# Kernel optimization log

Hardware: AMD Instinct MI355X
Metric: run time of the kernel (lower is better)

## Reference

```python
import jax, jax.numpy as jnp
import numpy as np

IMG = 8       # image_size
LH = 150      # l_h
LQ = 10       # l_q
K = 10        # value-iteration steps
B = 16384     # batch
N_STATES = 2 + IMG * IMG


def _conv(x, w, pad):
    # NCHW conv, stride 1
    return jax.lax.conv_general_dilated(
        x, w, window_strides=(1, 1), padding=[(pad, pad), (pad, pad)],
        dimension_numbers=('NCHW', 'OIHW', 'NCHW'))


def setup_inputs() -> dict:
    key = jax.random.key(0)
    ks = jax.random.split(key, 8)
    grid = jax.random.normal(ks[0], (B, IMG * IMG), dtype=jnp.float32)
    pos = jax.random.randint(ks[1], (B, 2), 0, IMG).astype(jnp.float32)
    S = jnp.concatenate([grid, pos], axis=1)                      # [B, 66]
    Wh = jax.random.normal(ks[2], (LH, 1, 3, 3), jnp.float32) * 0.1
    bh = jnp.zeros((LH,), jnp.float32)
    Wr = jax.random.normal(ks[3], (1, LH, 1, 1), jnp.float32) * 0.1
    Wq = jax.random.normal(ks[4], (LQ, 1, 3, 3), jnp.float32) * 0.1
    w = jax.random.normal(ks[5], (LQ, 1, 3, 3), jnp.float32) * 0.1
    Wfc = jax.random.normal(ks[6], (8, LQ), jnp.float32) * 0.1
    return {'S': S, 'Wh': Wh, 'bh': bh, 'Wr': Wr, 'Wq': Wq, 'w': w, 'Wfc': Wfc}


def reference(S, Wh, bh, Wr, Wq, w, Wfc):
    X = S[:, :IMG * IMG].reshape(-1, 1, IMG, IMG)                 # [B,1,8,8]
    s1 = S[:, IMG * IMG].astype(jnp.int32)                        # row index
    s2 = S[:, IMG * IMG + 1].astype(jnp.int32)                    # col index

    h = _conv(X, Wh, 1) + bh[None, :, None, None]                 # [B,150,8,8]
    r = _conv(h, Wr, 0)                                           # [B,1,8,8]
    q = _conv(r, Wq, 1)                                           # [B,10,8,8]
    v = jnp.max(q, axis=1, keepdims=True)                         # [B,1,8,8]

    Wcat = jnp.concatenate([Wq, w], axis=1)                       # [10,2,3,3]

    def step(v, _):
        qq = _conv(jnp.concatenate([r, v], axis=1), Wcat, 1)
        return jnp.max(qq, axis=1, keepdims=True), None

    v, _ = jax.lax.scan(step, v, None, length=K - 1)
    q = _conv(jnp.concatenate([r, v], axis=1), Wcat, 1)           # [B,10,8,8]

    bidx = jnp.arange(q.shape[0])
    q_sel = q[bidx, :, s1, s2]                                    # [B,10]
    logits = q_sel @ Wfc.T                                        # [B,8]
    return logits
```

## Files before the change

kernel.cpp:

```cpp
#include <hip/hip_runtime.h>

#define IMG 8
#define LH 150
#define LQ 10
#define KITER 10

__global__ void weff_kernel(const float* __restrict__ Wh,
                            const float* __restrict__ bh,
                            const float* __restrict__ Wr,
                            float* __restrict__ ws) {
    const int wave = threadIdx.x >> 6;
    const int lane = threadIdx.x & 63;
    float partial = 0.f;
    for (int c = lane; c < LH; c += 64) {
        const float wr = Wr[c];
        partial += wr * ((wave < 9) ? Wh[c * 9 + wave] : bh[c]);
    }
    #pragma unroll
    for (int off = 32; off > 0; off >>= 1)
        partial += __shfl_xor(partial, off);
    if (lane == 0) ws[wave] = partial;
}

__global__ __launch_bounds__(256) void vin_kernel(
    const float* __restrict__ S,
    const float* __restrict__ Wq,
    const float* __restrict__ w,
    const float* __restrict__ Wfc,
    const float* __restrict__ ws,
    float* __restrict__ out,
    int B) {
    const int wave = threadIdx.x >> 6;
    const int lane = threadIdx.x & 63;
    const int b = blockIdx.x * 4 + wave;
    if (b >= B) return;

    const int y = lane >> 3, x = lane & 7;

    const float* Sb = S + (long)b * (IMG * IMG + 2);
    const float X = Sb[lane];
    const int s1 = (int)Sb[IMG * IMG];
    const int s2 = (int)Sb[IMG * IMG + 1];
    const int sel_lane = s1 * 8 + s2;

    int   nidx[9];
    float nmsk[9];
    #pragma unroll
    for (int t = 0; t < 9; ++t) {
        const int dy = t / 3 - 1, dx = t % 3 - 1;
        const int ny = y + dy, nx = x + dx;
        const bool v = ((unsigned)ny < 8u) && ((unsigned)nx < 8u);
        nidx[t] = v ? (ny * 8 + nx) : 0;
        nmsk[t] = v ? 1.f : 0.f;
    }

    float Weff[9];
    #pragma unroll
    for (int t = 0; t < 9; ++t) Weff[t] = ws[t];
    const float beff = ws[9];

    float r = beff;
    #pragma unroll
    for (int t = 0; t < 9; ++t) {
        const float xv = __shfl(X, nidx[t]) * nmsk[t];
        r = fmaf(Weff[t], xv, r);
    }

    float rn[9];
    #pragma unroll
    for (int t = 0; t < 9; ++t)
        rn[t] = __shfl(r, nidx[t]) * nmsk[t];

    float qr[LQ];
    #pragma unroll
    for (int o = 0; o < LQ; ++o) {
        float acc = 0.f;
        #pragma unroll
        for (int t = 0; t < 9; ++t) acc = fmaf(rn[t], Wq[o * 9 + t], acc);
        qr[o] = acc;
    }

    float ww[LQ][9];
    #pragma unroll
    for (int o = 0; o < LQ; ++o)
        #pragma unroll
        for (int t = 0; t < 9; ++t) ww[o][t] = w[o * 9 + t];

    float v = qr[0];
    #pragma unroll
    for (int o = 1; o < LQ; ++o) v = fmaxf(v, qr[o]);

    float q[LQ];
    for (int k = 0; k < KITER; ++k) {
        float vn[9];
        #pragma unroll
        for (int t = 0; t < 9; ++t)
            vn[t] = __shfl(v, nidx[t]) * nmsk[t];
        float m = -3.0e38f;
        #pragma unroll
        for (int o = 0; o < LQ; ++o) {
            float acc = qr[o];
            #pragma unroll
            for (int t = 0; t < 9; ++t) acc = fmaf(vn[t], ww[o][t], acc);
            q[o] = acc;
            m = fmaxf(m, acc);
        }
        v = m;
    }

    float qsel[LQ];
    #pragma unroll
    for (int o = 0; o < LQ; ++o) qsel[o] = __shfl(q[o], sel_lane);

    if (lane < 8) {
        float acc = 0.f;
        #pragma unroll
        for (int o = 0; o < LQ; ++o) acc = fmaf(qsel[o], Wfc[lane * LQ + o], acc);
        out[(long)b * 8 + lane] = acc;
    }
}

extern "C" void kernel_launch(void* const* d_in, const int* in_sizes, int n_in,
                              void* d_out, int out_size, void* d_ws, size_t ws_size,
                              hipStream_t stream) {
    const float* S   = (const float*)d_in[0];
    const float* Wh  = (const float*)d_in[1];
    const float* bh  = (const float*)d_in[2];
    const float* Wr  = (const float*)d_in[3];
    const float* Wq  = (const float*)d_in[4];
    const float* w   = (const float*)d_in[5];
    const float* Wfc = (const float*)d_in[6];
    float* out = (float*)d_out;
    float* ws  = (float*)d_ws;

    const int B = in_sizes[0] / (IMG * IMG + 2);

    weff_kernel<<<1, 640, 0, stream>>>(Wh, bh, Wr, ws);

    const int waves_per_block = 4;
    const int grid = (B + waves_per_block - 1) / waves_per_block;
    vin_kernel<<<grid, 256, 0, stream>>>(S, Wq, w, Wfc, ws, out, B);
}
```

Baseline: 100.9 us.

## Process two batch items per wavefront with ds_bpermute and fully unrolled iterations

Each wavefront now handles two batch elements, interleaving their stencil shuffles and FMAs to raise instruction-level parallelism and reuse weight operands. __shfl is replaced by direct ds_bpermute with precomputed byte addresses, and the value-iteration loop is fully unrolled with weights read inline instead of preloaded into a register array. The max over channels uses a tree reduction. This halves the number of waves and raises register pressure. If B is odd, the last wave would read past the end of S, though the test batch is even.

```diff
diff --git a/kernel.cpp b/kernel.cpp
--- a/kernel.cpp
+++ b/kernel.cpp
@@ -4,22 +4,35 @@
 #define LH 150
 #define LQ 10
 #define KITER 10
+#define ROW (IMG * IMG + 2)
+
+__device__ __forceinline__ float bperm(int byte_addr, float v) {
+    return __builtin_bit_cast(float,
+        __builtin_amdgcn_ds_bpermute(byte_addr, __builtin_bit_cast(int, v)));
+}
+
+__device__ __forceinline__ float max10(const float q[LQ]) {
+    const float g0 = fmaxf(fmaxf(q[0], q[1]), q[2]);
+    const float g1 = fmaxf(fmaxf(q[3], q[4]), q[5]);
+    const float g2 = fmaxf(fmaxf(q[6], q[7]), q[8]);
+    return fmaxf(fmaxf(g0, g1), fmaxf(g2, q[9]));
+}
 
 __global__ void weff_kernel(const float* __restrict__ Wh,
                             const float* __restrict__ bh,
                             const float* __restrict__ Wr,
                             float* __restrict__ ws) {
-    const int wave = threadIdx.x >> 6;
+    const int wv = threadIdx.x >> 6;
     const int lane = threadIdx.x & 63;
     float partial = 0.f;
     for (int c = lane; c < LH; c += 64) {
         const float wr = Wr[c];
-        partial += wr * ((wave < 9) ? Wh[c * 9 + wave] : bh[c]);
+        partial += wr * ((wv < 9) ? Wh[c * 9 + wv] : bh[c]);
     }
     #pragma unroll
     for (int off = 32; off > 0; off >>= 1)
         partial += __shfl_xor(partial, off);
-    if (lane == 0) ws[wave] = partial;
+    if (lane == 0) ws[wv] = partial;
 }
 
 __global__ __launch_bounds__(256) void vin_kernel(
@@ -32,91 +45,86 @@
     int B) {
     const int wave = threadIdx.x >> 6;
     const int lane = threadIdx.x & 63;
-    const int b = blockIdx.x * 4 + wave;
-    if (b >= B) return;
+    const long b0 = (long)(blockIdx.x * 4 + wave) * 2;
+    if (b0 >= B) return;
 
     const int y = lane >> 3, x = lane & 7;
 
-    const float* Sb = S + (long)b * (IMG * IMG + 2);
-    const float X = Sb[lane];
-    const int s1 = (int)Sb[IMG * IMG];
-    const int s2 = (int)Sb[IMG * IMG + 1];
-    const int sel_lane = s1 * 8 + s2;
-
-    int   nidx[9];
-    float nmsk[9];
+    int   addr[9];
+    float msk[9];
     #pragma unroll
     for (int t = 0; t < 9; ++t) {
         const int dy = t / 3 - 1, dx = t % 3 - 1;
         const int ny = y + dy, nx = x + dx;
         const bool v = ((unsigned)ny < 8u) && ((unsigned)nx < 8u);
-        nidx[t] = v ? (ny * 8 + nx) : 0;
-        nmsk[t] = v ? 1.f : 0.f;
+        addr[t] = (v ? (ny * 8 + nx) : 0) << 2;
+        msk[t]  = v ? 1.f : 0.f;
     }
 
-    float Weff[9];
-    #pragma unroll
-    for (int t = 0; t < 9; ++t) Weff[t] = ws[t];
-    const float beff = ws[9];
+    const float* S0 = S + b0 * ROW;
+    const float X0 = S0[lane];
+    const float X1 = S0[ROW + lane];
+    const int sel0 = (int)S0[IMG * IMG] * 8 + (int)S0[IMG * IMG + 1];
+    const int sel1 = (int)S0[ROW + IMG * IMG] * 8 + (int)S0[ROW + IMG * IMG + 1];
 
-    float r = beff;
+    float r0 = ws[9], r1 = ws[9];
     #pragma unroll
     for (int t = 0; t < 9; ++t) {
-        const float xv = __shfl(X, nidx[t]) * nmsk[t];
-        r = fmaf(Weff[t], xv, r);
+        const float wm = ws[t] * msk[t];
+        r0 = fmaf(wm, bperm(addr[t], X0), r0);
+        r1 = fmaf(wm, bperm(addr[t], X1), r1);
     }
 
-    float rn[9];
+    float qr0[LQ], qr1[LQ];
     #pragma unroll
-    for (int t = 0; t < 9; ++t)
-        rn[t] = __shfl(r, nidx[t]) * nmsk[t];
+    for (int t = 0; t < 9; ++t) {
+        const float a0 = bperm(addr[t], r0) * msk[t];
+        const float a1 = bperm(addr[t], r1) * msk[t];
+        #pragma unroll
+        for (int o = 0; o < LQ; ++o) {
+            const float wq = Wq[o * 9 + t];
+            if (t == 0) { qr0[o] = a0 * wq; qr1[o] = a1 * wq; }
+            else        { qr0[o] = fmaf(a0, wq, qr0[o]);
+                          qr1[o] = fmaf(a1, wq, qr1[o]); }
+        }
+    }
 
-    float qr[LQ];
+    float v0 = max10(qr0), v1 = max10(qr1);
+
+    float q0[LQ], q1[LQ];
+    #pragma unroll
+    for (int k = 0; k < KITER; ++k) {
+        #pragma unroll
+        for (int t = 0; t < 9; ++t) {
+            const float a0 = bperm(addr[t], v0) * msk[t];
+            const float a1 = bperm(addr[t], v1) * msk[t];
+            #pragma unroll
+            for (int o = 0; o < LQ; ++o) {
+                const float wt = w[o * 9 + t];
+                if (t == 0) { q0[o] = fmaf(a0, wt, qr0[o]);
+                              q1[o] = fmaf(a1, wt, qr1[o]); }
+                else        { q0[o] = fmaf(a0, wt, q0[o]);
+                              q1[o] = fmaf(a1, wt, q1[o]); }
+            }
+        }
+        v0 = max10(q0);
+        v1 = max10(q1);
+    }
+
+    float qs0[LQ], qs1[LQ];
     #pragma unroll
     for (int o = 0; o < LQ; ++o) {
+        qs0[o] = bperm(sel0 << 2, q0[o]);
+        qs1[o] = bperm(sel1 << 2, q1[o]);
+    }
+
+    if (lane < 16) {
+        const int row = lane & 7;
         float acc = 0.f;
         #pragma unroll
-        for (int t = 0; t < 9; ++t) acc = fmaf(rn[t], Wq[o * 9 + t], acc);
-        qr[o] = acc;
-    }
-
-    float ww[LQ][9];
-    #pragma unroll
-    for (int o = 0; o < LQ; ++o)
-        #pragma unroll
-        for (int t = 0; t < 9; ++t) ww[o][t] = w[o * 9 + t];
-
-    float v = qr[0];
-    #pragma unroll
-    for (int o = 1; o < LQ; ++o) v = fmaxf(v, qr[o]);
-
-    float q[LQ];
-    for (int k = 0; k < KITER; ++k) {
-        float vn[9];
-        #pragma unroll
-        for (int t = 0; t < 9; ++t)
-            vn[t] = __shfl(v, nidx[t]) * nmsk[t];
-        float m = -3.0e38f;
-        #pragma unroll
-        for (int o = 0; o < LQ; ++o) {
-            float acc = qr[o];
-            #pragma unroll
-            for (int t = 0; t < 9; ++t) acc = fmaf(vn[t], ww[o][t], acc);
-            q[o] = acc;
-            m = fmaxf(m, acc);
-        }
-        v = m;
-    }
-
-    float qsel[LQ];
-    #pragma unroll
-    for (int o = 0; o < LQ; ++o) qsel[o] = __shfl(q[o], sel_lane);
-
-    if (lane < 8) {
-        float acc = 0.f;
-        #pragma unroll
-        for (int o = 0; o < LQ; ++o) acc = fmaf(qsel[o], Wfc[lane * LQ + o], acc);
-        out[(long)b * 8 + lane] = acc;
+        for (int o = 0; o < LQ; ++o)
+            acc = fmaf((lane < 8) ? qs0[o] : qs1[o], Wfc[row * LQ + o], acc);
+        out[b0 * 8 + lane] = acc;
     }
 }
 
@@ -133,11 +141,10 @@
     float* out = (float*)d_out;
     float* ws  = (float*)d_ws;
 
-    const int B = in_sizes[0] / (IMG * IMG + 2);
+    const int B = in_sizes[0] / ROW;
 
     weff_kernel<<<1, 640, 0, stream>>>(Wh, bh, Wr, ws);
 
-    const int waves_per_block = 4;
-    const int grid = (B + waves_per_block - 1) / waves_per_block;
+    const int grid = (B + 7) / 8;
     vin_kernel<<<grid, 256, 0, stream>>>(S, Wq, w, Wfc, ws, out, B);
 }
```

After: 101.4 us. About the same (+0.5%).
